# Optimization experiments

Measured on AMD Instinct MI355X. Metric: run time of the kernel, lower is better.

Reference implementation:

```python
import jax, jax.numpy as jnp
import numpy as np

U, I, J = 256, 512, 31          # nframes, n_actions, atom_max+1
E_IN, N_EMB, N_FIT = 3, 10, 32  # len(elements)+1, N_emb, N_fit
K = N_EMB // 4                  # slice size in the descriptor einsum


def setup_inputs() -> dict:
    key = jax.random.key(0)
    ks = jax.random.split(key, 12)
    s = 0.1
    return {
        "Sg": jax.random.normal(ks[0], (U, I, J, E_IN), jnp.float32),
        "R": jax.random.normal(ks[1], (U, I, J, 4), jnp.float32),
        # mlp_emb: Linear(3,10) -> ReLU -> Linear(10,10)  (weights stored [in,out])
        "W_emb1": jax.random.normal(ks[2], (E_IN, N_EMB), jnp.float32) * s,
        "b_emb1": jax.random.normal(ks[3], (N_EMB,), jnp.float32) * s,
        "W_emb2": jax.random.normal(ks[4], (N_EMB, N_EMB), jnp.float32) * s,
        "b_emb2": jax.random.normal(ks[5], (N_EMB,), jnp.float32) * s,
        # mlp_fit: Linear(20,32) -> ReLU -> Linear(32,32) -> ReLU -> Linear(32,1)
        "W_fit1": jax.random.normal(ks[6], (K * N_EMB, N_FIT), jnp.float32) * s,
        "b_fit1": jax.random.normal(ks[7], (N_FIT,), jnp.float32) * s,
        "W_fit2": jax.random.normal(ks[8], (N_FIT, N_FIT), jnp.float32) * s,
        "b_fit2": jax.random.normal(ks[9], (N_FIT,), jnp.float32) * s,
        "W_fit3": jax.random.normal(ks[10], (N_FIT, 1), jnp.float32) * s,
        "b_fit3": jax.random.normal(ks[11], (1,), jnp.float32) * s,
    }


def reference(Sg, R, W_emb1, b_emb1, W_emb2, b_emb2,
              W_fit1, b_fit1, W_fit2, b_fit2, W_fit3, b_fit3):
    # Embedding MLP on per-neighbor species/weight vectors: [u,i,j,3] -> [u,i,j,10]
    h = jnp.maximum(Sg @ W_emb1 + b_emb1, 0.0)
    Gmat = h @ W_emb2 + b_emb2
    # Descriptor: einsum('uijk,uijl,uiml,uimn->uikn') decomposed to avoid
    # materializing the full 4-way product; sums over both neighbor dims.
    T1 = jnp.einsum('uijk,uijl->uikl', Gmat[..., :K], R)   # [u,i,2,4]
    T2 = jnp.einsum('uiml,uimn->uiln', R, Gmat)            # [u,i,4,10]
    Dmat = jnp.einsum('uikl,uiln->uikn', T1, T2)           # [u,i,2,10]
    D = Dmat.reshape(U * I, K * N_EMB)
    # Fit MLP -> scalar Q per (frame, action)
    f = jnp.maximum(D @ W_fit1 + b_fit1, 0.0)
    f = jnp.maximum(f @ W_fit2 + b_fit2, 0.0)
    Q = f @ W_fit3 + b_fit3
    return Q.reshape(U, I, 1)
```

## Files before the change

kernel.cpp:

```cpp
#include <hip/hip_runtime.h>

constexpr int J_ = 31;
constexpr int UI = 131072;
constexpr size_t D_BYTES = (size_t)UI * 20 * 4;

constexpr int PPT   = 16;
constexpr int TILES = 4;
constexpr int SGB   = PPT * 93 * 4;
constexpr int SGPAD = 6144;
constexpr int NBLK1 = UI / (PPT * TILES);

typedef __attribute__((address_space(1))) const void g1void;
typedef __attribute__((address_space(3))) void s3void;

__device__ __forceinline__ float qsum(float x) {
    int a = __builtin_amdgcn_update_dpp(0, __float_as_int(x), 0xB1, 0xF, 0xF, true);
    x += __int_as_float(a);
    int b = __builtin_amdgcn_update_dpp(0, __float_as_int(x), 0x4E, 0xF, 0xF, true);
    x += __int_as_float(b);
    return x;
}

__global__ __launch_bounds__(64) void dqn_phase1(
    const float* __restrict__ Sg, const float* __restrict__ R,
    const float* __restrict__ W1, const float* __restrict__ b1,
    const float* __restrict__ W2, const float* __restrict__ b2,
    float* __restrict__ Dws)
{
    __shared__ float4 sbuf4[2 * SGPAD / 16];
    char* sb = reinterpret_cast<char*>(sbuf4);

    const int tid = threadIdx.x;
    const int lp  = tid >> 2;
    const int g   = tid & 3;

    float w10[10], w11[10], w12[10], c1w[10];
    #pragma unroll
    for (int p = 0; p < 10; ++p) {
        w10[p] = W1[p]; w11[p] = W1[10 + p]; w12[p] = W1[20 + p]; c1w[p] = b1[p];
    }

    auto STAGE = [&](int tile, int off) {
        const char* gS = reinterpret_cast<const char*>(Sg) + (size_t)tile * SGB;
        #pragma unroll
        for (int r = 0; r < 6; ++r) {
            int byte = r * 1024 + tid * 16;
            if (byte > SGB - 16) byte = SGB - 16;
            __builtin_amdgcn_global_load_lds((g1void*)(gS + byte),
                                             (s3void*)(sb + off + r * 1024),
                                             16, 0, 0);
        }
    };

    auto LOADR = [&](int tile, float4& r0, float4& r1, float4& r2, float4& r3,
                     float4& r4, float4& r5, float4& r6, float4& r7) {
        const float4* rv = reinterpret_cast<const float4*>(
            R + (size_t)(tile * PPT + lp) * 124);
        r0 = rv[g];      r1 = rv[4 + g];  r2 = rv[8 + g];  r3 = rv[12 + g];
        r4 = rv[16 + g]; r5 = rv[20 + g]; r6 = rv[24 + g];
        int jt = 28 + g;
        r7 = rv[jt < J_ ? jt : (J_ - 1)];
    };

    auto COMPUTE = [&](int off, int tileIdx,
                       float4 r0, float4 r1, float4 r2, float4 r3,
                       float4 r4, float4 r5, float4 r6, float4 r7) {
        const float* sgL = reinterpret_cast<const float*>(sb + off) + lp * 93;

        float M0[10], M1[10], M2[10], M3[10];
        float4 Rs = {0.f, 0.f, 0.f, 0.f};
        #pragma unroll
        for (int p = 0; p < 10; ++p) { M0[p]=0.f; M1[p]=0.f; M2[p]=0.f; M3[p]=0.f; }

        auto PROC = [&](int j, const float4& r4v) {
            float s0 = sgL[j * 3 + 0];
            float s1 = sgL[j * 3 + 1];
            float s2 = sgL[j * 3 + 2];
            #pragma unroll
            for (int p = 0; p < 10; ++p) {
                float t = c1w[p] + s0 * w10[p] + s1 * w11[p] + s2 * w12[p];
                t = t > 0.f ? t : 0.f;
                M0[p] += r4v.x * t;
                M1[p] += r4v.y * t;
                M2[p] += r4v.z * t;
                M3[p] += r4v.w * t;
            }
            Rs.x += r4v.x; Rs.y += r4v.y; Rs.z += r4v.z; Rs.w += r4v.w;
        };

        PROC(g,      r0); PROC(4 + g,  r1); PROC(8 + g,  r2); PROC(12 + g, r3);
        PROC(16 + g, r4); PROC(20 + g, r5); PROC(24 + g, r6);
        {
            float m = (g < 3) ? 1.f : 0.f;
            float4 rm = {r7.x * m, r7.y * m, r7.z * m, r7.w * m};
            PROC(28 + g, rm);
        }

        #pragma unroll
        for (int p = 0; p < 10; ++p) {
            M0[p] = qsum(M0[p]); M1[p] = qsum(M1[p]);
            M2[p] = qsum(M2[p]); M3[p] = qsum(M3[p]);
        }
        Rs.x = qsum(Rs.x); Rs.y = qsum(Rs.y); Rs.z = qsum(Rs.z); Rs.w = qsum(Rs.w);

        float Mg[10];
        #pragma unroll
        for (int p = 0; p < 10; ++p)
            Mg[p] = (g == 0) ? M0[p] : (g == 1) ? M1[p] : (g == 2) ? M2[p] : M3[p];
        float Rsg = (g == 0) ? Rs.x : (g == 1) ? Rs.y : (g == 2) ? Rs.z : Rs.w;

        float T2g[10];
        #pragma unroll
        for (int n = 0; n < 10; ++n) T2g[n] = Rsg * b2[n];
        #pragma unroll
        for (int p = 0; p < 10; ++p) {
            float m = Mg[p];
            #pragma unroll
            for (int n = 0; n < 10; ++n) T2g[n] += m * W2[p * 10 + n];
        }

        float D[20];
        #pragma unroll
        for (int k = 0; k < 2; ++k)
            #pragma unroll
            for (int n = 0; n < 10; ++n) D[k * 10 + n] = T2g[k] * T2g[n];
        #pragma unroll
        for (int t = 0; t < 20; ++t) D[t] = qsum(D[t]);

        float* dw = Dws + tileIdx * PPT + lp;
        if (g == 0) {
            dw[0 * UI] = D[0];  dw[1 * UI] = D[1];  dw[2 * UI] = D[2];
            dw[3 * UI] = D[3];  dw[4 * UI] = D[4];
        } else if (g == 1) {
            dw[5 * UI] = D[5];  dw[6 * UI] = D[6];  dw[7 * UI] = D[7];
            dw[8 * UI] = D[8];  dw[9 * UI] = D[9];
        } else if (g == 2) {
            dw[10 * UI] = D[10]; dw[11 * UI] = D[11]; dw[12 * UI] = D[12];
            dw[13 * UI] = D[13]; dw[14 * UI] = D[14];
        } else {
            dw[15 * UI] = D[15]; dw[16 * UI] = D[16]; dw[17 * UI] = D[17];
            dw[18 * UI] = D[18]; dw[19 * UI] = D[19];
        }
    };

    const int t0 = blockIdx.x * TILES;
    float4 pA0,pA1,pA2,pA3,pA4,pA5,pA6,pA7;
    float4 pB0,pB1,pB2,pB3,pB4,pB5,pB6,pB7;

    STAGE(t0 + 0, 0);     LOADR(t0 + 0, pA0,pA1,pA2,pA3,pA4,pA5,pA6,pA7);
    STAGE(t0 + 1, SGPAD); LOADR(t0 + 1, pB0,pB1,pB2,pB3,pB4,pB5,pB6,pB7);
    asm volatile("s_waitcnt vmcnt(14)" ::: "memory");
    __builtin_amdgcn_sched_barrier(0);
    COMPUTE(0, t0 + 0, pA0,pA1,pA2,pA3,pA4,pA5,pA6,pA7);

    STAGE(t0 + 2, 0);     LOADR(t0 + 2, pA0,pA1,pA2,pA3,pA4,pA5,pA6,pA7);
    asm volatile("s_waitcnt vmcnt(14)" ::: "memory");
    __builtin_amdgcn_sched_barrier(0);
    COMPUTE(SGPAD, t0 + 1, pB0,pB1,pB2,pB3,pB4,pB5,pB6,pB7);

    STAGE(t0 + 3, SGPAD); LOADR(t0 + 3, pB0,pB1,pB2,pB3,pB4,pB5,pB6,pB7);
    asm volatile("s_waitcnt vmcnt(14)" ::: "memory");
    __builtin_amdgcn_sched_barrier(0);
    COMPUTE(0, t0 + 2, pA0,pA1,pA2,pA3,pA4,pA5,pA6,pA7);

    asm volatile("s_waitcnt vmcnt(0)" ::: "memory");
    __builtin_amdgcn_sched_barrier(0);
    COMPUTE(SGPAD, t0 + 3, pB0,pB1,pB2,pB3,pB4,pB5,pB6,pB7);
}

__global__ __launch_bounds__(256) void dqn_phase2(
    const float* __restrict__ Dws,
    const float* __restrict__ Wf1, const float* __restrict__ bf1,
    const float* __restrict__ Wf2, const float* __restrict__ bf2,
    const float* __restrict__ Wf3, const float* __restrict__ bf3,
    float* __restrict__ out)
{
    __shared__ float4 wlds4[448];
    const int tid = threadIdx.x;

    {
        if (tid < 160) wlds4[tid] = reinterpret_cast<const float4*>(Wf1)[tid];
        wlds4[160 + tid] = reinterpret_cast<const float4*>(Wf2)[tid];
        if (tid < 8)       wlds4[416 + tid]        = reinterpret_cast<const float4*>(bf1)[tid];
        else if (tid < 16) wlds4[424 + (tid - 8)]  = reinterpret_cast<const float4*>(bf2)[tid - 8];
        else if (tid < 24) wlds4[432 + (tid - 16)] = reinterpret_cast<const float4*>(Wf3)[tid - 16];
        else if (tid == 24) { reinterpret_cast<float*>(wlds4)[1760] = bf3[0]; }
    }
    __syncthreads();

    const int gt   = blockIdx.x * 256 + tid;
    const int pair = gt >> 2;
    const int g    = gt & 3;

    float D[20];
    #pragma unroll
    for (int t = 0; t < 20; ++t) D[t] = Dws[(size_t)t * UI + pair];

    const float* wl = reinterpret_cast<const float*>(wlds4);

    float F[8];
    {
        const float4* b4 = reinterpret_cast<const float4*>(wl + 1664 + g * 8);
        float4 x = b4[0], y = b4[1];
        F[0]=x.x; F[1]=x.y; F[2]=x.z; F[3]=x.w; F[4]=y.x; F[5]=y.y; F[6]=y.z; F[7]=y.w;
    }
    #pragma unroll
    for (int kk = 0; kk < 20; ++kk) {
        float d = D[kk];
        const float4* w4 = reinterpret_cast<const float4*>(wl + kk * 32 + g * 8);
        float4 wa = w4[0], wb = w4[1];
        F[0] += d * wa.x; F[1] += d * wa.y; F[2] += d * wa.z; F[3] += d * wa.w;
        F[4] += d * wb.x; F[5] += d * wb.y; F[6] += d * wb.z; F[7] += d * wb.w;
    }
    #pragma unroll
    for (int i = 0; i < 8; ++i) F[i] = F[i] > 0.f ? F[i] : 0.f;

    float P[8];
    #pragma unroll
    for (int i = 0; i < 8; ++i) P[i] = __shfl_xor(F[i], 1);
    const bool odd = (g & 1);
    float lo[16];
    #pragma unroll
    for (int i = 0; i < 8; ++i) {
        lo[i]     = odd ? P[i] : F[i];
        lo[8 + i] = odd ? F[i] : P[i];
    }
    float hi[16];
    #pragma unroll
    for (int i = 0; i < 16; ++i) hi[i] = __shfl_xor(lo[i], 2);
    const bool up = (g & 2);
    float f1a[32];
    #pragma unroll
    for (int i = 0; i < 16; ++i) {
        f1a[i]      = up ? hi[i] : lo[i];
        f1a[16 + i] = up ? lo[i] : hi[i];
    }

    float G[8];
    {
        const float4* b4 = reinterpret_cast<const float4*>(wl + 1696 + g * 8);
        float4 x = b4[0], y = b4[1];
        G[0]=x.x; G[1]=x.y; G[2]=x.z; G[3]=x.w; G[4]=y.x; G[5]=y.y; G[6]=y.z; G[7]=y.w;
    }
    #pragma unroll
    for (int kk = 0; kk < 32; ++kk) {
        float d = f1a[kk];
        const float4* w4 = reinterpret_cast<const float4*>(wl + 640 + kk * 32 + g * 8);
        float4 wa = w4[0], wb = w4[1];
        G[0] += d * wa.x; G[1] += d * wa.y; G[2] += d * wa.z; G[3] += d * wa.w;
        G[4] += d * wb.x; G[5] += d * wb.y; G[6] += d * wb.z; G[7] += d * wb.w;
    }
    #pragma unroll
    for (int i = 0; i < 8; ++i) G[i] = G[i] > 0.f ? G[i] : 0.f;

    float qp;
    {
        const float4* w4 = reinterpret_cast<const float4*>(wl + 1728 + g * 8);
        float4 wa = w4[0], wb = w4[1];
        qp = G[0]*wa.x + G[1]*wa.y + G[2]*wa.z + G[3]*wa.w
           + G[4]*wb.x + G[5]*wb.y + G[6]*wb.z + G[7]*wb.w;
    }
    qp += __shfl_xor(qp, 1);
    qp += __shfl_xor(qp, 2);
    float q = qp + wl[1760];

    if (g == 0) out[pair] = q;
}

struct Nb1 { float s0, s1, s2; float4 r; };
__device__ __forceinline__ Nb1 load_nb1(const float* __restrict__ sg,
                                        const float* __restrict__ rr, int j) {
    Nb1 d;
    d.s0 = sg[j * 3 + 0]; d.s1 = sg[j * 3 + 1]; d.s2 = sg[j * 3 + 2];
    d.r = *reinterpret_cast<const float4*>(rr + j * 4);
    return d;
}
__global__ __launch_bounds__(256, 2) void dqn_fused_fb(
    const float* __restrict__ Sg,  const float* __restrict__ R,
    const float* __restrict__ W1,  const float* __restrict__ b1,
    const float* __restrict__ W2,  const float* __restrict__ b2,
    const float* __restrict__ Wf1, const float* __restrict__ bf1,
    const float* __restrict__ Wf2, const float* __restrict__ bf2,
    const float* __restrict__ Wf3, const float* __restrict__ bf3,
    float* __restrict__ out)
{
    const int pair = blockIdx.x * 256 + threadIdx.x;
    const float* sg = Sg + (size_t)pair * (J_ * 3);
    const float* rr = R  + (size_t)pair * (J_ * 4);
    float w1[3][10], c1[10];
    #pragma unroll
    for (int k = 0; k < 3; ++k)
        #pragma unroll
        for (int p = 0; p < 10; ++p) w1[k][p] = W1[k * 10 + p];
    #pragma unroll
    for (int p = 0; p < 10; ++p) c1[p] = b1[p];
    float M[4][10]; float Rs[4] = {0.f,0.f,0.f,0.f};
    #pragma unroll
    for (int l = 0; l < 4; ++l)
        #pragma unroll
        for (int p = 0; p < 10; ++p) M[l][p] = 0.f;
    #pragma unroll 1
    for (int j = 0; j < J_; ++j) {
        Nb1 nb = load_nb1(sg, rr, j);
        float h[10];
        #pragma unroll
        for (int p = 0; p < 10; ++p) {
            float t = c1[p] + nb.s0*w1[0][p] + nb.s1*w1[1][p] + nb.s2*w1[2][p];
            h[p] = t > 0.f ? t : 0.f;
        }
        Rs[0]+=nb.r.x; Rs[1]+=nb.r.y; Rs[2]+=nb.r.z; Rs[3]+=nb.r.w;
        #pragma unroll
        for (int p = 0; p < 10; ++p) {
            M[0][p]+=nb.r.x*h[p]; M[1][p]+=nb.r.y*h[p];
            M[2][p]+=nb.r.z*h[p]; M[3][p]+=nb.r.w*h[p];
        }
    }
    float T2[4][10];
    #pragma unroll
    for (int l = 0; l < 4; ++l)
        #pragma unroll
        for (int n = 0; n < 10; ++n) T2[l][n] = Rs[l] * b2[n];
    #pragma unroll
    for (int p = 0; p < 10; ++p) {
        #pragma unroll
        for (int l = 0; l < 4; ++l) {
            float m = M[l][p];
            #pragma unroll
            for (int n = 0; n < 10; ++n) T2[l][n] += m * W2[p * 10 + n];
        }
    }
    float D[20];
    #pragma unroll
    for (int k = 0; k < 2; ++k)
        #pragma unroll
        for (int n = 0; n < 10; ++n)
            D[k*10+n] = T2[0][k]*T2[0][n] + T2[1][k]*T2[1][n]
                      + T2[2][k]*T2[2][n] + T2[3][k]*T2[3][n];
    float f1[32];
    #pragma unroll
    for (int o = 0; o < 32; ++o) f1[o] = bf1[o];
    #pragma unroll
    for (int kk = 0; kk < 20; ++kk) {
        const float4* wrow = reinterpret_cast<const float4*>(Wf1 + kk * 32);
        float d = D[kk];
        #pragma unroll
        for (int v = 0; v < 8; ++v) {
            float4 w = wrow[v];
            f1[4*v+0]+=d*w.x; f1[4*v+1]+=d*w.y; f1[4*v+2]+=d*w.z; f1[4*v+3]+=d*w.w;
        }
    }
    #pragma unroll
    for (int o = 0; o < 32; ++o) f1[o] = f1[o] > 0.f ? f1[o] : 0.f;
    float f2[32];
    #pragma unroll
    for (int o = 0; o < 32; ++o) f2[o] = bf2[o];
    #pragma unroll
    for (int kk = 0; kk < 32; ++kk) {
        const float4* wrow = reinterpret_cast<const float4*>(Wf2 + kk * 32);
        float d = f1[kk];
        #pragma unroll
        for (int v = 0; v < 8; ++v) {
            float4 w = wrow[v];
            f2[4*v+0]+=d*w.x; f2[4*v+1]+=d*w.y; f2[4*v+2]+=d*w.z; f2[4*v+3]+=d*w.w;
        }
    }
    #pragma unroll
    for (int o = 0; o < 32; ++o) f2[o] = f2[o] > 0.f ? f2[o] : 0.f;
    float q = bf3[0];
    #pragma unroll
    for (int o = 0; o < 32; o += 4) {
        float4 w = *reinterpret_cast<const float4*>(Wf3 + o);
        q += f2[o+0]*w.x + f2[o+1]*w.y + f2[o+2]*w.z + f2[o+3]*w.w;
    }
    out[pair] = q;
}

extern "C" void kernel_launch(void* const* d_in, const int* in_sizes, int n_in,
                              void* d_out, int out_size, void* d_ws, size_t ws_size,
                              hipStream_t stream) {
    const float* Sg  = (const float*)d_in[0];
    const float* R   = (const float*)d_in[1];
    const float* W1  = (const float*)d_in[2];
    const float* b1  = (const float*)d_in[3];
    const float* W2  = (const float*)d_in[4];
    const float* b2  = (const float*)d_in[5];
    const float* Wf1 = (const float*)d_in[6];
    const float* bf1 = (const float*)d_in[7];
    const float* Wf2 = (const float*)d_in[8];
    const float* bf2 = (const float*)d_in[9];
    const float* Wf3 = (const float*)d_in[10];
    const float* bf3 = (const float*)d_in[11];
    float* out = (float*)d_out;

    if (ws_size >= D_BYTES) {
        float* Dws = (float*)d_ws;
        dqn_phase1<<<dim3(NBLK1), dim3(64), 0, stream>>>(
            Sg, R, W1, b1, W2, b2, Dws);
        dqn_phase2<<<dim3((UI * 4) / 256), dim3(256), 0, stream>>>(
            Dws, Wf1, bf1, Wf2, bf2, Wf3, bf3, out);
    } else {
        dqn_fused_fb<<<dim3(UI / 256), dim3(256), 0, stream>>>(
            Sg, R, W1, b1, W2, b2, Wf1, bf1, Wf2, bf2, Wf3, bf3, out);
    }
}
```

Before: 52.52 us.

## Halve tiles per block, stage W2/b2 in LDS, branchless D stores

Each phase-1 block now processes two tiles instead of four, doubling the grid for more parallelism and shortening the per-block pipeline. W2 and b2 are copied into shared memory once per block instead of being read through global/scalar loads inside compute. The four-way branch for writing D is replaced by select-based value choice and a single computed store pointer, which removes divergence. The trade-off is less double-buffer overlap per block, and the vmcnt(5) wait count now has to match the changed number of outstanding loads, since the W2/b2 staging loads also count toward vmcnt.

Result: faster. 46.45 us (-11.6%).

```diff
diff --git a/kernel.cpp b/kernel.cpp
--- a/kernel.cpp
+++ b/kernel.cpp
@@ -5,10 +5,11 @@
 constexpr size_t D_BYTES = (size_t)UI * 20 * 4;
 
 constexpr int PPT   = 16;
-constexpr int TILES = 4;
+constexpr int TILES = 2;
 constexpr int SGB   = PPT * 93 * 4;
 constexpr int SGPAD = 6144;
 constexpr int NBLK1 = UI / (PPT * TILES);
+constexpr int WOFF  = 2 * SGPAD / 4;
 
 typedef __attribute__((address_space(1))) const void g1void;
 typedef __attribute__((address_space(3))) void s3void;
@@ -27,12 +28,16 @@
     const float* __restrict__ W2, const float* __restrict__ b2,
     float* __restrict__ Dws)
 {
-    __shared__ float4 sbuf4[2 * SGPAD / 16];
-    char* sb = reinterpret_cast<char*>(sbuf4);
+    __shared__ float4 sbuf4[(2 * SGPAD + 512) / 16];
+    char*  sb  = reinterpret_cast<char*>(sbuf4);
+    float* wl2 = reinterpret_cast<float*>(sbuf4) + WOFF;
 
     const int tid = threadIdx.x;
     const int lp  = tid >> 2;
     const int g   = tid & 3;
+
+    for (int i = tid; i < 100; i += 64) wl2[i] = W2[i];
+    if (tid < 10) wl2[100 + tid] = b2[tid];
 
     float w10[10], w11[10], w12[10], c1w[10];
     #pragma unroll
@@ -111,12 +116,12 @@
 
         float T2g[10];
         #pragma unroll
-        for (int n = 0; n < 10; ++n) T2g[n] = Rsg * b2[n];
+        for (int n = 0; n < 10; ++n) T2g[n] = Rsg * wl2[100 + n];
         #pragma unroll
         for (int p = 0; p < 10; ++p) {
             float m = Mg[p];
             #pragma unroll
-            for (int n = 0; n < 10; ++n) T2g[n] += m * W2[p * 10 + n];
+            for (int n = 0; n < 10; ++n) T2g[n] += m * wl2[p * 10 + n];
         }
 
         float D[20];
@@ -127,20 +132,14 @@
         #pragma unroll
         for (int t = 0; t < 20; ++t) D[t] = qsum(D[t]);
 
-        float* dw = Dws + tileIdx * PPT + lp;
-        if (g == 0) {
-            dw[0 * UI] = D[0];  dw[1 * UI] = D[1];  dw[2 * UI] = D[2];
-            dw[3 * UI] = D[3];  dw[4 * UI] = D[4];
-        } else if (g == 1) {
-            dw[5 * UI] = D[5];  dw[6 * UI] = D[6];  dw[7 * UI] = D[7];
-            dw[8 * UI] = D[8];  dw[9 * UI] = D[9];
-        } else if (g == 2) {
-            dw[10 * UI] = D[10]; dw[11 * UI] = D[11]; dw[12 * UI] = D[12];
-            dw[13 * UI] = D[13]; dw[14 * UI] = D[14];
-        } else {
-            dw[15 * UI] = D[15]; dw[16 * UI] = D[16]; dw[17 * UI] = D[17];
-            dw[18 * UI] = D[18]; dw[19 * UI] = D[19];
-        }
+        float s0 = (g == 0) ? D[0] : (g == 1) ? D[5]  : (g == 2) ? D[10] : D[15];
+        float s1 = (g == 0) ? D[1] : (g == 1) ? D[6]  : (g == 2) ? D[11] : D[16];
+        float s2 = (g == 0) ? D[2] : (g == 1) ? D[7]  : (g == 2) ? D[12] : D[17];
+        float s3 = (g == 0) ? D[3] : (g == 1) ? D[8]  : (g == 2) ? D[13] : D[18];
+        float s4 = (g == 0) ? D[4] : (g == 1) ? D[9]  : (g == 2) ? D[14] : D[19];
+        float* dw = Dws + (size_t)(g * 5) * UI + tileIdx * PPT + lp;
+        dw[0 * UI] = s0; dw[1 * UI] = s1; dw[2 * UI] = s2;
+        dw[3 * UI] = s3; dw[4 * UI] = s4;
     };
 
     const int t0 = blockIdx.x * TILES;
@@ -152,20 +151,9 @@
     asm volatile("s_waitcnt vmcnt(14)" ::: "memory");
     __builtin_amdgcn_sched_barrier(0);
     COMPUTE(0, t0 + 0, pA0,pA1,pA2,pA3,pA4,pA5,pA6,pA7);
-
-    STAGE(t0 + 2, 0);     LOADR(t0 + 2, pA0,pA1,pA2,pA3,pA4,pA5,pA6,pA7);
-    asm volatile("s_waitcnt vmcnt(14)" ::: "memory");
+    asm volatile("s_waitcnt vmcnt(5)" ::: "memory");
     __builtin_amdgcn_sched_barrier(0);
     COMPUTE(SGPAD, t0 + 1, pB0,pB1,pB2,pB3,pB4,pB5,pB6,pB7);
-
-    STAGE(t0 + 3, SGPAD); LOADR(t0 + 3, pB0,pB1,pB2,pB3,pB4,pB5,pB6,pB7);
-    asm volatile("s_waitcnt vmcnt(14)" ::: "memory");
-    __builtin_amdgcn_sched_barrier(0);
-    COMPUTE(0, t0 + 2, pA0,pA1,pA2,pA3,pA4,pA5,pA6,pA7);
-
-    asm volatile("s_waitcnt vmcnt(0)" ::: "memory");
-    __builtin_amdgcn_sched_barrier(0);
-    COMPUTE(SGPAD, t0 + 3, pB0,pB1,pB2,pB3,pB4,pB5,pB6,pB7);
 }
 
 __global__ __launch_bounds__(256) void dqn_phase2(
```
